# Optimization experiments

Hardware: AMD Instinct MI355X
Metric: run time of the kernel (lower is better)

The kernel has to match this reference:

```python
import jax, jax.numpy as jnp
import numpy as np

DIM = 768
HEADS = 12
HEAD_DIM = DIM // HEADS
SCALE = HEAD_DIM ** (-0.5)


def setup_inputs() -> dict:
    key = jax.random.key(0)
    k1, k2, k3, k4 = jax.random.split(key, 4)
    B, N = 2, 48 * 48
    x = jax.random.normal(k1, (B, N, DIM), dtype=jnp.float32)
    qkv_w = jax.random.normal(k2, (3 * DIM, DIM), dtype=jnp.float32) * (DIM ** -0.5)
    proj_w = jax.random.normal(k3, (DIM, DIM), dtype=jnp.float32) * (DIM ** -0.5)
    proj_b = jax.random.normal(k4, (DIM,), dtype=jnp.float32) * 0.02
    return {"x": x, "H": 48, "W": 48, "qkv_w": qkv_w, "proj_w": proj_w, "proj_b": proj_b}


def reference(x, H, W, qkv_w, proj_w, proj_b):
    B, N, C = x.shape
    h, d = HEADS, HEAD_DIM
    # qkv linear (no bias): [B,N,3C], then split into per-head q,k,v [B,h,N,d]
    qkv = jnp.einsum('bnc,fc->bnf', x, qkv_w)
    qkv = qkv.reshape(B, N, 3, h, d).transpose(2, 0, 3, 1, 4)
    q, k, v = qkv[0], qkv[1], qkv[2]
    attn = jnp.einsum('bhnd,bhmd->bhnm', q, k) * SCALE  # [B,h,N,N]
    attn = jax.nn.softmax(attn, axis=-1)
    out = jnp.einsum('bhnm,bhmd->bhnd', attn, v)  # [B,h,N,d]
    out = out.transpose(0, 2, 1, 3).reshape(B, N, C)
    out = jnp.einsum('bnc,fc->bnf', out, proj_w) + proj_b
    return out
```

## Files before the change

kernel.cpp:

```cpp
#include <hip/hip_runtime.h>

#define B_    2
#define N_    2304
#define C_    768
#define HEADS 12
#define D_    64
#define F3    2304
#define M_    (B_*N_)
#define SPLITS 3
#define KSPAN (N_/SPLITS)
#define QSCALE 0.18033688011112042f

typedef __attribute__((ext_vector_type(8)))  short bfrag;
typedef __attribute__((ext_vector_type(4)))  float ffrag;
typedef __attribute__((ext_vector_type(16))) float ffrag16;
typedef __attribute__((ext_vector_type(4)))  unsigned ufrag;
typedef __attribute__((ext_vector_type(2)))  unsigned uint2v;

__device__ __forceinline__ short f2bf(float f) {
    unsigned u = __float_as_uint(f);
    u += 0x7fff + ((u >> 16) & 1);
    return (short)(u >> 16);
}

__device__ __forceinline__ void gl2lds16(const void* g, void* l) {
    __builtin_amdgcn_global_load_lds(
        (const __attribute__((address_space(1))) void*)g,
        (__attribute__((address_space(3))) void*)l, 16, 0, 0);
}

__device__ __forceinline__ unsigned pktrunc(float a, float b) {
    return __builtin_amdgcn_perm(__float_as_uint(a), __float_as_uint(b),
                                 0x03020706u);
}

__device__ __forceinline__ float btrunc(float a) {
    return __uint_as_float(__float_as_uint(a) & 0xffff0000u);
}

__global__ __launch_bounds__(256) void cast_all(const float* __restrict__ x,
                                                const float* __restrict__ qw,
                                                const float* __restrict__ pw,
                                                short* __restrict__ dst) {
    const int nx4 = (M_*C_)/4, nq4 = (F3*C_)/4, np4 = (C_*C_)/4;
    int i = blockIdx.x * 256 + threadIdx.x;
    if (i >= nx4 + nq4 + np4) return;
    const float* src; int off;
    if (i < nx4)            { src = x;  off = i; }
    else if (i < nx4 + nq4) { src = qw; off = i - nx4; }
    else                    { src = pw; off = i - nx4 - nq4; }
    float4 v = ((const float4*)src)[off];
    short4 o;
    o.x = f2bf(v.x); o.y = f2bf(v.y); o.z = f2bf(v.z); o.w = f2bf(v.w);
    ((short4*)dst)[i] = o;
}

__global__ __launch_bounds__(256) void qkv_gemm(const short* __restrict__ xb,
                                                const short* __restrict__ wb,
                                                short* __restrict__ Qb,
                                                short* __restrict__ Kb,
                                                short* __restrict__ Vtb) {
    __shared__ short As[2][128*32];
    __shared__ short Bs[2][128*32];
    const int t = threadIdx.x;
    const int w = t >> 6, lane = t & 63;
    const int quad = lane >> 4, l15 = lane & 15;
    const int wr = w >> 1, wc = w & 1;

    const int nwg = gridDim.x * gridDim.y;
    const int bid = blockIdx.y * gridDim.x + blockIdx.x;
    const int swz = (bid & 7) * (nwg >> 3) + (bid >> 3);
    const int m0 = (swz / gridDim.x) * 128, f0 = (swz % gridDim.x) * 128;

    const int srow = lane >> 2;
    const int skk  = (lane & 3) * 8;

    ffrag acc[4][4] = {};

    #pragma unroll
    for (int r = 0; r < 2; ++r) {
        int seg = r*4 + w;
        int row = seg*16 + srow;
        gl2lds16(xb + (size_t)(m0+row)*C_ + skk, As[0] + seg*512);
        gl2lds16(wb + (size_t)(f0+row)*C_ + skk, Bs[0] + seg*512);
    }
    __syncthreads();

    const int NKT = C_/32;
    for (int kt = 0; kt < NKT; ++kt) {
        const int cur = kt & 1;
        if (kt + 1 < NKT) {
            const int k0n = (kt+1)*32;
            #pragma unroll
            for (int r = 0; r < 2; ++r) {
                int seg = r*4 + w;
                int row = seg*16 + srow;
                gl2lds16(xb + (size_t)(m0+row)*C_ + k0n + skk, As[cur^1] + seg*512);
                gl2lds16(wb + (size_t)(f0+row)*C_ + k0n + skk, Bs[cur^1] + seg*512);
            }
        }
        bfrag af[4], bf[4];
        #pragma unroll
        for (int i = 0; i < 4; ++i)
            af[i] = *(const bfrag*)(As[cur] + (wr*64 + i*16 + l15)*32 + quad*8);
        #pragma unroll
        for (int j = 0; j < 4; ++j)
            bf[j] = *(const bfrag*)(Bs[cur] + (wc*64 + j*16 + l15)*32 + quad*8);
        #pragma unroll
        for (int i = 0; i < 4; ++i)
            #pragma unroll
            for (int j = 0; j < 4; ++j)
                acc[i][j] = __builtin_amdgcn_mfma_f32_16x16x32_bf16(af[i], bf[j], acc[i][j], 0, 0, 0);
        __syncthreads();
    }

    const int b   = m0 / N_;
    const int seg = f0 + wc*64;
    const int which = seg / C_;
    const int head  = (seg - which*C_) >> 6;
    const int bh    = b*HEADS + head;
    const int nbase = (m0 - b*N_) + wr*64 + quad*4;

    if (which == 0) {
        #pragma unroll
        for (int i = 0; i < 4; ++i) {
            int n0 = nbase + i*16;
            #pragma unroll
            for (int j = 0; j < 4; ++j) {
                int d = j*16 + l15;
                #pragma unroll
                for (int r = 0; r < 4; ++r)
                    Qb[((size_t)bh*N_ + n0 + r)*D_ + d] = f2bf(acc[i][j][r] * QSCALE);
            }
        }
    } else if (which == 1) {
        #pragma unroll
        for (int i = 0; i < 4; ++i) {
            int n0 = nbase + i*16;
            #pragma unroll
            for (int j = 0; j < 4; ++j) {
                int d = j*16 + l15;
                #pragma unroll
                for (int r = 0; r < 4; ++r)
                    Kb[((size_t)bh*N_ + n0 + r)*D_ + d] = f2bf(acc[i][j][r]);
            }
        }
    } else {
        #pragma unroll
        for (int i = 0; i < 4; ++i) {
            int n0 = nbase + i*16;
            #pragma unroll
            for (int j = 0; j < 4; ++j) {
                int d = j*16 + l15;
                short4 vv;
                vv.x = f2bf(acc[i][j][0]);
                vv.y = f2bf(acc[i][j][1]);
                vv.z = f2bf(acc[i][j][2]);
                vv.w = f2bf(acc[i][j][3]);
                *(short4*)(Vtb + ((size_t)bh*D_ + d)*N_ + n0) = vv;
            }
        }
    }
}

__global__ __launch_bounds__(256, 4) void attn_mfma(const short* __restrict__ Qb,
                                                    const short* __restrict__ Kb,
                                                    const short* __restrict__ Vtb,
                                                    float* __restrict__ Opart,
                                                    float* __restrict__ lpart) {
    __shared__ short lds[16384];
    const int t = threadIdx.x;
    const int w = t >> 6, lane = t & 63;
    const int l31 = lane & 31, hi = lane >> 5;
    const int bh = blockIdx.x, q0 = blockIdx.y * 128;
    const int split = blockIdx.z;
    const int kbase = split * KSPAN;
    const size_t base = (size_t)bh * N_ * D_;
    const int lrow = lane >> 3;
    const int lc   = (lane & 7) ^ lrow;

    short* Qs = lds + 8192;

    #pragma unroll
    for (int r = 0; r < 4; ++r) {
        int s = r*4 + w;
        gl2lds16(Qb + base + (size_t)(q0 + s*8 + lrow)*D_ + lc*8, Qs + s*512);
    }
    #pragma unroll
    for (int r = 0; r < 2; ++r) {
        int s = r*4 + w;
        int row = s*8 + lrow;
        gl2lds16(Kb  + base + (size_t)(kbase+row)*D_ + lc*8,    lds + s*512);
        gl2lds16(Vtb + (size_t)(bh*D_ + row)*N_ + kbase + lc*8, lds + 4096 + s*512);
    }
    __syncthreads();

    bfrag qf[4];
    {
        int row = w*32 + l31, r7 = row & 7;
        #pragma unroll
        for (int kc = 0; kc < 4; ++kc)
            qf[kc] = *(const bfrag*)(Qs + row*64 + ((kc*2 + hi) ^ r7)*8);
    }
    __syncthreads();

    ffrag16 oacc[2];
    #pragma unroll
    for (int r = 0; r < 16; ++r) { oacc[0][r] = 0.f; oacc[1][r] = 0.f; }
    float llane = 0.f;

    const int NT = KSPAN / 64;
    for (int ti = 0; ti < NT; ++ti) {
        const int cur = ti & 1;
        const short* Kc = lds + cur*8192;
        const short* Vc = Kc + 4096;

        if (ti + 1 < NT) {
            short* Kn = lds + (cur^1)*8192;
            const int k0n = kbase + (ti+1)*64;
            #pragma unroll
            for (int r = 0; r < 2; ++r) {
                int s = r*4 + w;
                int row = s*8 + lrow;
                gl2lds16(Kb  + base + (size_t)(k0n+row)*D_ + lc*8,    Kn + s*512);
                gl2lds16(Vtb + (size_t)(bh*D_ + row)*N_ + k0n + lc*8, Kn + 4096 + s*512);
            }
        }

        ufrag pfr[4];
        #pragma unroll
        for (int kt = 0; kt < 2; ++kt) {
            ffrag16 s;
            #pragma unroll
            for (int r = 0; r < 16; ++r) s[r] = 0.f;
            int row = kt*32 + l31, r7 = row & 7;
            __builtin_amdgcn_s_setprio(1);
            #pragma unroll
            for (int kc = 0; kc < 4; ++kc) {
                bfrag kf = *(const bfrag*)(Kc + row*64 + ((kc*2 + hi) ^ r7)*8);
                s = __builtin_amdgcn_mfma_f32_32x32x16_bf16(kf, qf[kc], s, 0, 0, 0);
            }
            __builtin_amdgcn_s_setprio(0);
            #pragma unroll
            for (int r = 0; r < 16; ++r)
                s[r] = __builtin_amdgcn_exp2f(s[r]);
            {
                float t0 = 0.f, t1 = 0.f;
                #pragma unroll
                for (int r = 0; r < 16; r += 2) {
                    t0 += btrunc(s[r]);
                    t1 += btrunc(s[r+1]);
                }
                llane += t0 + t1;
            }
            unsigned q01_0 = pktrunc(s[0],  s[1]),  q23_0 = pktrunc(s[2],  s[3]);
            unsigned q01_1 = pktrunc(s[4],  s[5]),  q23_1 = pktrunc(s[6],  s[7]);
            unsigned q01_2 = pktrunc(s[8],  s[9]),  q23_2 = pktrunc(s[10], s[11]);
            unsigned q01_3 = pktrunc(s[12], s[13]), q23_3 = pktrunc(s[14], s[15]);
            uint2v e0 = __builtin_amdgcn_permlane32_swap(q01_0, q01_1, false, false);
            uint2v e1 = __builtin_amdgcn_permlane32_swap(q23_0, q23_1, false, false);
            uint2v e2 = __builtin_amdgcn_permlane32_swap(q01_2, q01_3, false, false);
            uint2v e3 = __builtin_amdgcn_permlane32_swap(q23_2, q23_3, false, false);
            ufrag lo, hif;
            lo[0]  = e0[0]; lo[1]  = e1[0]; lo[2]  = e0[1]; lo[3]  = e1[1];
            hif[0] = e2[0]; hif[1] = e3[0]; hif[2] = e2[1]; hif[3] = e3[1];
            pfr[kt*2]     = lo;
            pfr[kt*2 + 1] = hif;
        }

        __builtin_amdgcn_s_setprio(1);
        #pragma unroll
        for (int kc = 0; kc < 4; ++kc) {
            bfrag pf = __builtin_bit_cast(bfrag, pfr[kc]);
            #pragma unroll
            for (int dt = 0; dt < 2; ++dt) {
                int row = dt*32 + l31, r7 = row & 7;
                bfrag vf = *(const bfrag*)(Vc + row*64 + ((kc*2 + hi) ^ r7)*8);
                oacc[dt] = __builtin_amdgcn_mfma_f32_32x32x16_bf16(pf, vf, oacc[dt], 0, 0, 0);
            }
        }
        __builtin_amdgcn_s_setprio(0);
        __syncthreads();
    }

    const int b = bh / HEADS, head = bh - b*HEADS;
    float* Op = Opart + (size_t)split * M_ * C_;
    float* lp = lpart + (size_t)split * (B_*HEADS) * N_;

    {
        float lpart_other = __shfl_xor(llane, 32, 64);
        float ltot = llane + lpart_other;
        if (hi == 0)
            lp[bh*N_ + q0 + w*32 + l31] = ltot;
    }

    #pragma unroll
    for (int dt = 0; dt < 2; ++dt)
        #pragma unroll
        for (int r = 0; r < 16; ++r) {
            int n = q0 + w*32 + (r & 3) + 8*(r >> 2) + 4*hi;
            int c = head*D_ + dt*32 + l31;
            Op[((size_t)b*N_ + n)*C_ + c] = oacc[dt][r];
        }
}

__global__ __launch_bounds__(256) void attn_merge(const float* __restrict__ Opart,
                                                  const float* __restrict__ lpart,
                                                  short* __restrict__ Ob) {
    int i = blockIdx.x * 256 + threadIdx.x;
    int m = i / (C_/4);
    int c = (i - m*(C_/4)) * 4;
    int b = m / N_, n = m - b*N_;
    int bh = b*HEADS + (c >> 6);
    const int LP = (B_*HEADS)*N_;
    float4 o0 = ((const float4*)Opart)[i];
    float4 o1 = ((const float4*)(Opart + (size_t)M_*C_))[i];
    float4 o2 = ((const float4*)(Opart + 2*(size_t)M_*C_))[i];
    float l = lpart[bh*N_ + n] + lpart[LP + bh*N_ + n] + lpart[2*LP + bh*N_ + n];
    float inv = 1.f / l;
    short4 o;
    o.x = f2bf((o0.x + o1.x + o2.x) * inv);
    o.y = f2bf((o0.y + o1.y + o2.y) * inv);
    o.z = f2bf((o0.z + o1.z + o2.z) * inv);
    o.w = f2bf((o0.w + o1.w + o2.w) * inv);
    ((short4*)Ob)[i] = o;
}

__global__ __launch_bounds__(256) void proj_gemm(const short* __restrict__ Ab,
                                                 const short* __restrict__ wb,
                                                 const float* __restrict__ bias,
                                                 float* __restrict__ out) {
    __shared__ short As[2][128*32];
    __shared__ short Bs[2][128*32];
    const int t = threadIdx.x;
    const int w = t >> 6, lane = t & 63;
    const int quad = lane >> 4, l15 = lane & 15;
    const int wr = w >> 1, wc = w & 1;

    const int nwg = gridDim.x * gridDim.y;
    const int bid = blockIdx.y * gridDim.x + blockIdx.x;
    const int swz = (bid & 7) * (nwg >> 3) + (bid >> 3);
    const int m0 = (swz / gridDim.x) * 128, f0 = (swz % gridDim.x) * 128;

    const int srow = lane >> 2;
    const int skk  = (lane & 3) * 8;

    ffrag acc[4][4] = {};

    #pragma unroll
    for (int r = 0; r < 2; ++r) {
        int seg = r*4 + w;
        int row = seg*16 + srow;
        gl2lds16(Ab + (size_t)(m0+row)*C_ + skk, As[0] + seg*512);
        gl2lds16(wb + (size_t)(f0+row)*C_ + skk, Bs[0] + seg*512);
    }
    __syncthreads();

    const int NKT = C_/32;
    for (int kt = 0; kt < NKT; ++kt) {
        const int cur = kt & 1;
        if (kt + 1 < NKT) {
            const int k0n = (kt+1)*32;
            #pragma unroll
            for (int r = 0; r < 2; ++r) {
                int seg = r*4 + w;
                int row = seg*16 + srow;
                gl2lds16(Ab + (size_t)(m0+row)*C_ + k0n + skk, As[cur^1] + seg*512);
                gl2lds16(wb + (size_t)(f0+row)*C_ + k0n + skk, Bs[cur^1] + seg*512);
            }
        }
        bfrag af[4], bf[4];
        #pragma unroll
        for (int i = 0; i < 4; ++i)
            af[i] = *(const bfrag*)(As[cur] + (wr*64 + i*16 + l15)*32 + quad*8);
        #pragma unroll
        for (int j = 0; j < 4; ++j)
            bf[j] = *(const bfrag*)(Bs[cur] + (wc*64 + j*16 + l15)*32 + quad*8);
        #pragma unroll
        for (int i = 0; i < 4; ++i)
            #pragma unroll
            for (int j = 0; j < 4; ++j)
                acc[i][j] = __builtin_amdgcn_mfma_f32_16x16x32_bf16(af[i], bf[j], acc[i][j], 0, 0, 0);
        __syncthreads();
    }

    #pragma unroll
    for (int i = 0; i < 4; ++i) {
        int mbase = m0 + wr*64 + i*16 + quad*4;
        #pragma unroll
        for (int j = 0; j < 4; ++j) {
            int f = f0 + wc*64 + j*16 + l15;
            float bv = bias[f];
            #pragma unroll
            for (int r = 0; r < 4; ++r)
                out[(size_t)(mbase + r)*C_ + f] = acc[i][j][r] + bv;
        }
    }
}

extern "C" void kernel_launch(void* const* d_in, const int* in_sizes, int n_in,
                              void* d_out, int out_size, void* d_ws, size_t ws_size,
                              hipStream_t stream) {
    const float* x      = (const float*)d_in[0];
    const float* qkv_w  = (const float*)d_in[3];
    const float* proj_w = (const float*)d_in[4];
    const float* proj_b = (const float*)d_in[5];
    float* out = (float*)d_out;

    const size_t nx = (size_t)M_ * C_;
    const size_t nq = (size_t)F3 * C_;
    const size_t np = (size_t)C_ * C_;
    short* xb  = (short*)d_ws;
    short* qwb = xb  + nx;
    short* pwb = qwb + nq;
    short* Qb  = pwb + np;
    short* Kb  = Qb  + nx;
    short* Vtb = Kb  + nx;
    short* Ob  = Vtb + nx;
    float* Opart = (float*)(Ob + nx);
    float* lpart = Opart + (size_t)SPLITS * M_ * C_;

    const int ncast4 = (int)((nx + nq + np) / 4);
    cast_all<<<dim3((ncast4 + 255)/256), 256, 0, stream>>>(x, qkv_w, proj_w, xb);

    qkv_gemm<<<dim3(F3/128, M_/128), 256, 0, stream>>>(xb, qwb, Qb, Kb, Vtb);
    attn_mfma<<<dim3(B_*HEADS, N_/128, SPLITS), 256, 0, stream>>>(Qb, Kb, Vtb, Opart, lpart);
    attn_merge<<<dim3(((int)(nx/4) + 255)/256), 256, 0, stream>>>(Opart, lpart, Ob);
    proj_gemm<<<dim3(C_/128, M_/128), 256, 0, stream>>>(Ob, pwb, proj_b, out);
}
```

Before: 194.0 us.

## Keep next-tile loads in flight with partial vmcnt waits; use two key splits

The full __syncthreads (which waits for all outstanding global-to-LDS loads) is replaced in the QKV GEMM, attention and projection loops with explicit s_waitcnt vmcnt(4)/vmcnt(0) plus a raw s_barrier. The current tile's loads complete while the prefetch of the next tile stays in flight across the barrier, overlapping memory with compute. Separately, the attention key dimension is split two ways instead of three, which halves merge traffic but halves the extra parallelism from splitting. The hand-written vmcnt counts rely on the compiler not reordering or adding other vector memory ops, which is fragile.

```diff
diff --git a/kernel.cpp b/kernel.cpp
--- a/kernel.cpp
+++ b/kernel.cpp
@@ -7,7 +7,7 @@
 #define D_    64
 #define F3    2304
 #define M_    (B_*N_)
-#define SPLITS 3
+#define SPLITS 2
 #define KSPAN (N_/SPLITS)
 #define QSCALE 0.18033688011112042f
 
@@ -28,6 +28,9 @@
         (const __attribute__((address_space(1))) void*)g,
         (__attribute__((address_space(3))) void*)l, 16, 0, 0);
 }
+
+__device__ __forceinline__ void wait_vm4() { asm volatile("s_waitcnt vmcnt(4)" ::: "memory"); }
+__device__ __forceinline__ void wait_vm0() { asm volatile("s_waitcnt vmcnt(0)" ::: "memory"); }
 
 __device__ __forceinline__ unsigned pktrunc(float a, float b) {
     return __builtin_amdgcn_perm(__float_as_uint(a), __float_as_uint(b),
@@ -84,7 +87,6 @@
         gl2lds16(xb + (size_t)(m0+row)*C_ + skk, As[0] + seg*512);
         gl2lds16(wb + (size_t)(f0+row)*C_ + skk, Bs[0] + seg*512);
     }
-    __syncthreads();
 
     const int NKT = C_/32;
     for (int kt = 0; kt < NKT; ++kt) {
@@ -98,7 +100,12 @@
                 gl2lds16(xb + (size_t)(m0+row)*C_ + k0n + skk, As[cur^1] + seg*512);
                 gl2lds16(wb + (size_t)(f0+row)*C_ + k0n + skk, Bs[cur^1] + seg*512);
             }
-        }
+            wait_vm4();
+        } else {
+            wait_vm0();
+        }
+        __builtin_amdgcn_s_barrier();
+
         bfrag af[4], bf[4];
         #pragma unroll
         for (int i = 0; i < 4; ++i)
@@ -111,7 +118,7 @@
             #pragma unroll
             for (int j = 0; j < 4; ++j)
                 acc[i][j] = __builtin_amdgcn_mfma_f32_16x16x32_bf16(af[i], bf[j], acc[i][j], 0, 0, 0);
-        __syncthreads();
+        __builtin_amdgcn_s_barrier();
     }
 
     const int b   = m0 / N_;
@@ -225,7 +232,11 @@
                 gl2lds16(Kb  + base + (size_t)(k0n+row)*D_ + lc*8,    Kn + s*512);
                 gl2lds16(Vtb + (size_t)(bh*D_ + row)*N_ + k0n + lc*8, Kn + 4096 + s*512);
             }
-        }
+            wait_vm4();
+        } else {
+            wait_vm0();
+        }
+        __builtin_amdgcn_s_barrier();
 
         ufrag pfr[4];
         #pragma unroll
@@ -280,7 +291,7 @@
             }
         }
         __builtin_amdgcn_s_setprio(0);
-        __syncthreads();
+        __builtin_amdgcn_s_barrier();
     }
 
     const int b = bh / HEADS, head = bh - b*HEADS;
@@ -312,17 +323,15 @@
     int c = (i - m*(C_/4)) * 4;
     int b = m / N_, n = m - b*N_;
     int bh = b*HEADS + (c >> 6);
-    const int LP = (B_*HEADS)*N_;
     float4 o0 = ((const float4*)Opart)[i];
     float4 o1 = ((const float4*)(Opart + (size_t)M_*C_))[i];
-    float4 o2 = ((const float4*)(Opart + 2*(size_t)M_*C_))[i];
-    float l = lpart[bh*N_ + n] + lpart[LP + bh*N_ + n] + lpart[2*LP + bh*N_ + n];
+    float l = lpart[bh*N_ + n] + lpart[(B_*HEADS)*N_ + bh*N_ + n];
     float inv = 1.f / l;
     short4 o;
-    o.x = f2bf((o0.x + o1.x + o2.x) * inv);
-    o.y = f2bf((o0.y + o1.y + o2.y) * inv);
-    o.z = f2bf((o0.z + o1.z + o2.z) * inv);
-    o.w = f2bf((o0.w + o1.w + o2.w) * inv);
+    o.x = f2bf((o0.x + o1.x) * inv);
+    o.y = f2bf((o0.y + o1.y) * inv);
+    o.z = f2bf((o0.z + o1.z) * inv);
+    o.w = f2bf((o0.w + o1.w) * inv);
     ((short4*)Ob)[i] = o;
 }
 
@@ -354,7 +363,6 @@
         gl2lds16(Ab + (size_t)(m0+row)*C_ + skk, As[0] + seg*512);
         gl2lds16(wb + (size_t)(f0+row)*C_ + skk, Bs[0] + seg*512);
     }
-    __syncthreads();
 
     const int NKT = C_/32;
     for (int kt = 0; kt < NKT; ++kt) {
@@ -368,7 +376,12 @@
                 gl2lds16(Ab + (size_t)(m0+row)*C_ + k0n + skk, As[cur^1] + seg*512);
                 gl2lds16(wb + (size_t)(f0+row)*C_ + k0n + skk, Bs[cur^1] + seg*512);
             }
-        }
+            wait_vm4();
+        } else {
+            wait_vm0();
+        }
+        __builtin_amdgcn_s_barrier();
+
         bfrag af[4], bf[4];
         #pragma unroll
         for (int i = 0; i < 4; ++i)
@@ -381,7 +394,7 @@
             #pragma unroll
             for (int j = 0; j < 4; ++j)
                 acc[i][j] = __builtin_amdgcn_mfma_f32_16x16x32_bf16(af[i], bf[j], acc[i][j], 0, 0, 0);
-        __syncthreads();
+        __builtin_amdgcn_s_barrier();
     }
 
     #pragma unroll
```

After: 193.6 us. Within noise of the previous version (-0.2%).
